# Performance work log

Measured on AMD Instinct MI355X. Metric: run time of the kernel, lower is better.

The kernel has to match this reference:

```python
import jax, jax.numpy as jnp
import numpy as np

N_LAYERS = 6
N_HEADS = 8
HIDDEN = 512
FILTER = 2048
KSIZE = 3
WINDOW = 10
DK = HIDDEN // N_HEADS


def _rel_to_abs(x):
    # x: [b, h, l, 2l-1] -> [b, h, l, l]
    b, h, l, _ = x.shape
    x = jnp.pad(x, ((0, 0), (0, 0), (0, 0), (0, 1)))
    x = x.reshape(b, h, l * 2 * l)
    x = jnp.pad(x, ((0, 0), (0, 0), (0, l - 1)))
    return x.reshape(b, h, l + 1, 2 * l - 1)[:, :, :l, l - 1:]


def _abs_to_rel(x):
    # x: [b, h, l, l] -> [b, h, l, 2l-1]
    b, h, l, _ = x.shape
    x = jnp.pad(x, ((0, 0), (0, 0), (0, 0), (0, l - 1)))
    x = x.reshape(b, h, l * l + l * (l - 1))
    x = jnp.pad(x, ((0, 0), (0, 0), (l, 0)))
    return x.reshape(b, h, l, 2 * l)[:, :, :, 1:]


def _get_rel_emb(emb, length):
    # emb: [1, 2w+1, dk] -> [1, 2*length-1, dk]  (static python ints)
    pad = max(length - (WINDOW + 1), 0)
    s = max(WINDOW + 1 - length, 0)
    e = s + 2 * length - 1
    emb = jnp.pad(emb, ((0, 0), (pad, pad), (0, 0)))
    return emb[:, s:e]


def _conv1x1(x, w, b):
    # x: [B, Cin, T], w: [Cout, Cin] -> [B, Cout, T]
    return jnp.einsum('oc,bct->bot', w, x) + b[None, :, None]


def _conv1d_same(x, w, b):
    # x: [B, Cin, T], w: [Cout, Cin, K], same padding (pad_l=(K-1)//2, pad_r=K//2)
    x = jnp.pad(x, ((0, 0), (0, 0), ((KSIZE - 1) // 2, KSIZE // 2)))
    y = jax.lax.conv_general_dilated(x, w, (1,), 'VALID',
                                     dimension_numbers=('NCH', 'OIH', 'NCH'))
    return y + b[None, :, None]


def _layer_norm(x, g, b):
    # normalize over channel axis (axis=1), eps=1e-5 (VITS LayerNorm)
    m = jnp.mean(x, axis=1, keepdims=True)
    v = jnp.var(x, axis=1, keepdims=True)
    return (x - m) * jax.lax.rsqrt(v + 1e-5) * g[None, :, None] + b[None, :, None]


def _mha(x, attn_mask, Wq, bq, Wk, bk, Wv, bv, Wo, bo, erk, erv):
    B, C, T = x.shape
    q = _conv1x1(x, Wq, bq)
    k = _conv1x1(x, Wk, bk)
    v = _conv1x1(x, Wv, bv)
    # [B, C, T] -> [B, H, T, Dk]
    def split_heads(t):
        return t.reshape(B, N_HEADS, DK, T).transpose(0, 1, 3, 2)
    q, k, v = split_heads(q), split_heads(k), split_heads(v)
    scale = 1.0 / np.sqrt(DK).astype(np.float32)
    scores = jnp.einsum('bhtd,bhsd->bhts', q * scale, k)
    # relative position logits
    rel_k = _get_rel_emb(erk, T)[0]                       # [2T-1, Dk]
    rel_logits = jnp.einsum('bhtd,rd->bhtr', q * scale, rel_k)
    scores = scores + _rel_to_abs(rel_logits)
    scores = jnp.where(attn_mask == 0, -1e4, scores)
    p = jax.nn.softmax(scores, axis=-1)
    out = jnp.einsum('bhts,bhsd->bhtd', p, v)
    rel_v = _get_rel_emb(erv, T)[0]                       # [2T-1, Dk]
    out = out + jnp.einsum('bhtr,rd->bhtd', _abs_to_rel(p), rel_v)
    out = out.transpose(0, 1, 3, 2).reshape(B, C, T)
    return _conv1x1(out, Wo, bo)


def _ffn(x, x_mask, W1, bf1, W2, bf2):
    y = _conv1d_same(x * x_mask, W1, bf1)
    y = jax.nn.relu(y)
    y = _conv1d_same(y * x_mask, W2, bf2)
    return y * x_mask


def reference(x, x_mask, Wq, bq, Wk, bk, Wv, bv, Wo, bo, erk, erv,
              g1, b1, g2, b2, W1, bf1, W2, bf2):
    attn_mask = x_mask[:, :, None, :] * x_mask[:, :, :, None]  # [B,1,T,T]
    x = x * x_mask
    for i in range(N_LAYERS):
        y = _mha(x, attn_mask, Wq[i], bq[i], Wk[i], bk[i], Wv[i], bv[i],
                 Wo[i], bo[i], erk[i], erv[i])
        x = _layer_norm(x + y, g1[i], b1[i])
        y = _ffn(x, x_mask, W1[i], bf1[i], W2[i], bf2[i])
        x = _layer_norm(x + y, g2[i], b2[i])
    return x * x_mask


def setup_inputs() -> dict:
    key = jax.random.key(0)
    ks = jax.random.split(key, 20)
    B, T = 8, 512
    xavier = lambda k, sh, fan: jax.random.normal(k, sh, jnp.float32) * np.sqrt(2.0 / fan).astype(np.float32)
    rel_std = DK ** -0.5
    return {
        'x': jax.random.normal(ks[0], (B, HIDDEN, T), jnp.float32),
        'x_mask': jnp.ones((B, 1, T), jnp.float32),
        'Wq': xavier(ks[1], (N_LAYERS, HIDDEN, HIDDEN), 2 * HIDDEN),
        'bq': jnp.zeros((N_LAYERS, HIDDEN), jnp.float32),
        'Wk': xavier(ks[2], (N_LAYERS, HIDDEN, HIDDEN), 2 * HIDDEN),
        'bk': jnp.zeros((N_LAYERS, HIDDEN), jnp.float32),
        'Wv': xavier(ks[3], (N_LAYERS, HIDDEN, HIDDEN), 2 * HIDDEN),
        'bv': jnp.zeros((N_LAYERS, HIDDEN), jnp.float32),
        'Wo': xavier(ks[4], (N_LAYERS, HIDDEN, HIDDEN), 2 * HIDDEN),
        'bo': jnp.zeros((N_LAYERS, HIDDEN), jnp.float32),
        'erk': jax.random.normal(ks[5], (N_LAYERS, 1, 2 * WINDOW + 1, DK), jnp.float32) * rel_std,
        'erv': jax.random.normal(ks[6], (N_LAYERS, 1, 2 * WINDOW + 1, DK), jnp.float32) * rel_std,
        'g1': jnp.ones((N_LAYERS, HIDDEN), jnp.float32),
        'b1': jnp.zeros((N_LAYERS, HIDDEN), jnp.float32),
        'g2': jnp.ones((N_LAYERS, HIDDEN), jnp.float32),
        'b2': jnp.zeros((N_LAYERS, HIDDEN), jnp.float32),
        'W1': jax.random.normal(ks[7], (N_LAYERS, FILTER, HIDDEN, KSIZE), jnp.float32) * np.sqrt(1.0 / (HIDDEN * KSIZE)).astype(np.float32),
        'bf1': jnp.zeros((N_LAYERS, FILTER), jnp.float32),
        'W2': jax.random.normal(ks[8], (N_LAYERS, HIDDEN, FILTER, KSIZE), jnp.float32) * np.sqrt(1.0 / (FILTER * KSIZE)).astype(np.float32),
        'bf2': jnp.zeros((N_LAYERS, HIDDEN), jnp.float32),
    }
```

## Files before the change

kernel.cpp:

```cpp
#include <hip/hip_runtime.h>


#define NLAYERS 6
#define BB 8
#define TT 512
#define CC 512
#define FF 2048
#define HH 8
#define DKK 64
#define WW 10

static_assert(CC == HH * DKK, "");

typedef __attribute__((ext_vector_type(8))) short short8;
typedef __attribute__((ext_vector_type(4))) float f32x4;
typedef unsigned short ushort;

#define BCTS ((size_t)BB * CC * TT)

__device__ __forceinline__ ushort f2bs(float f) {
    unsigned u = __float_as_uint(f);
    u = (u + 0x7FFFu + ((u >> 16) & 1u)) >> 16;
    return (ushort)u;
}
__device__ __forceinline__ float bf2f(ushort u) {
    return __uint_as_float(((unsigned)u) << 16);
}
__device__ __forceinline__ float wave_sum(float v) {
    #pragma unroll
    for (int off = 32; off > 0; off >>= 1) v += __shfl_xor(v, off, 64);
    return v;
}

__global__ __launch_bounds__(256) void init_trans(const float* __restrict__ in,
                                                  const float* __restrict__ mask,
                                                  float* __restrict__ xf,
                                                  ushort* __restrict__ xt) {
    __shared__ float tile[32][33];
    const int t0 = blockIdx.x * 32;
    const int c0 = blockIdx.y * 32;
    const int b = blockIdx.z;
    const int col = threadIdx.x & 31;
    const int row = threadIdx.x >> 5;
    const float* src = in + ((size_t)b * CC + c0) * TT + t0;
    #pragma unroll
    for (int r = 0; r < 32; r += 8)
        tile[row + r][col] = src[(size_t)(row + r) * TT + col];
    __syncthreads();
    #pragma unroll
    for (int r = 0; r < 32; r += 8) {
        const int t = t0 + row + r;
        const float mv = mask[b * TT + t];
        const float v = tile[col][row + r] * mv;
        const size_t idx = ((size_t)(b * TT) + t) * CC + c0 + col;
        xf[idx] = v;
        xt[idx] = f2bs(v);
    }
}

__global__ __launch_bounds__(256) void final_kernel(const float* __restrict__ xf,
                                                    const float* __restrict__ mask,
                                                    float* __restrict__ out) {
    __shared__ float tile[32][33];
    const int t0 = blockIdx.x * 32;
    const int c0 = blockIdx.y * 32;
    const int b = blockIdx.z;
    const int col = threadIdx.x & 31;
    const int row = threadIdx.x >> 5;
    #pragma unroll
    for (int r = 0; r < 32; r += 8)
        tile[row + r][col] = xf[((size_t)(b * TT) + t0 + row + r) * CC + c0 + col];
    __syncthreads();
    #pragma unroll
    for (int r = 0; r < 32; r += 8) {
        const int c = c0 + row + r;
        const int t = t0 + col;
        out[((size_t)b * CC + c) * TT + t] = tile[col][row + r] * mask[b * TT + t];
    }
}

__global__ __launch_bounds__(256) void wcvt_layer(const float* __restrict__ Wq,
                                                  const float* __restrict__ Wk,
                                                  const float* __restrict__ Wv,
                                                  const float* __restrict__ bq,
                                                  const float* __restrict__ bk,
                                                  const float* __restrict__ bv,
                                                  const float* __restrict__ Wo,
                                                  const float* __restrict__ W1,
                                                  const float* __restrict__ W2,
                                                  ushort* __restrict__ Wqkv,
                                                  float* __restrict__ bqkv,
                                                  ushort* __restrict__ Wot,
                                                  ushort* __restrict__ W1t,
                                                  ushort* __restrict__ W2t) {
    size_t i = (size_t)blockIdx.x * 256 + threadIdx.x;
    if (i < 1536)
        bqkv[i] = (i < 512) ? bq[i] : (i < 1024) ? bk[i - 512] : bv[i - 1024];
    if (i < 786432) {
        const int o = (int)(i >> 9), c = (int)(i & 511);
        const float* src = (o < 512) ? Wq : (o < 1024) ? Wk : Wv;
        Wqkv[i] = f2bs(src[(size_t)(o & 511) * 512 + c]);
        return;
    }
    i -= 786432;
    if (i < 262144) { Wot[i] = f2bs(Wo[i]); return; }
    i -= 262144;
    if (i < 3145728) {
        const int c = (int)(i & 511);
        const int o = (int)((i >> 9) & 2047);
        const int tap = (int)(i >> 20);
        W1t[i] = f2bs(W1[((size_t)o * 512 + c) * 3 + tap]);
        return;
    }
    i -= 3145728;
    if (i < 3145728) {
        const int c = (int)(i & 2047);
        const int o = (int)((i >> 11) & 511);
        const int tap = (int)(i >> 20);
        W2t[i] = f2bs(W2[((size_t)o * 2048 + c) * 3 + tap]);
    }
}

template <int MODE, int TN>
__global__ __launch_bounds__(256) void gemm128(const ushort* __restrict__ Wt,
                                               const float* __restrict__ bias,
                                               const ushort* __restrict__ Xin,
                                               void* __restrict__ Out,
                                               const float* __restrict__ mask,
                                               int O, int K, int taps, int kcs) {
    const int blk = blockIdx.x;
    const int b = blk >> 2;
    const int t0 = (blk & 3) * 128;
    const int o0 = blockIdx.y * TN;
    const int tid = threadIdx.x;
    const int wid = tid >> 6, lane = tid & 63, ln = lane & 15, q = lane >> 4;
    constexpr int MF = (TN == 128) ? 4 : 2;
    const int msub = (TN == 128) ? (wid & 1) * 64 : wid * 32;
    const int nsub = (TN == 128) ? (wid >> 1) * 64 : 0;

    __shared__ ushort Xs[128][40];
    __shared__ ushort Ws[TN][40];

    f32x4 acc[MF][4] = {};

    const int KC = K >> 5;
    const int NI = taps * KC;
    const int kcm = KC - 1;

    const int rx = tid >> 1;
    const int cx = (tid & 1) << 4;
    const int rw = (TN == 128) ? (tid >> 1) : (tid >> 2);
    const int cw = (TN == 128) ? ((tid & 1) << 4) : ((tid & 3) << 3);

    uint4 xr0, xr1, wr0, wr1;
    const uint4 zero = make_uint4(0u, 0u, 0u, 0u);

    auto load = [&](int it) {
        const int tap = it >> kcs;
        const int c0 = (it & kcm) << 5;
        const int shift = (taps > 1) ? (tap - 1) : 0;
        const int tt = t0 + rx + shift;
        const bool okt = (tt >= 0) && (tt < TT);
        const ushort* xp = Xin + ((size_t)(b * TT + (okt ? tt : 0)) * K + c0 + cx);
        xr0 = okt ? *(const uint4*)xp : zero;
        xr1 = okt ? *(const uint4*)(xp + 8) : zero;
        const ushort* wp = Wt + ((size_t)(tap * O + o0 + rw) * K + c0 + cw);
        wr0 = *(const uint4*)wp;
        if (TN == 128) wr1 = *(const uint4*)(wp + 8);
    };

    load(0);
    for (int it = 0; it < NI; ++it) {
        __syncthreads();
        *(uint4*)&Xs[rx][cx] = xr0;
        *(uint4*)&Xs[rx][cx + 8] = xr1;
        *(uint4*)&Ws[rw][cw] = wr0;
        if (TN == 128) *(uint4*)&Ws[rw][cw + 8] = wr1;
        if (it + 1 < NI) load(it + 1);
        __syncthreads();
        short8 afr[MF], bfr[4];
        #pragma unroll
        for (int mi = 0; mi < MF; ++mi)
            afr[mi] = *(const short8*)&Xs[msub + mi * 16 + ln][q * 8];
        #pragma unroll
        for (int ni = 0; ni < 4; ++ni)
            bfr[ni] = *(const short8*)&Ws[nsub + ni * 16 + ln][q * 8];
        #pragma unroll
        for (int mi = 0; mi < MF; ++mi)
            #pragma unroll
            for (int ni = 0; ni < 4; ++ni)
                acc[mi][ni] = __builtin_amdgcn_mfma_f32_16x16x32_bf16(
                    afr[mi], bfr[ni], acc[mi][ni], 0, 0, 0);
    }

    #pragma unroll
    for (int ni = 0; ni < 4; ++ni) {
        const int o = o0 + nsub + ni * 16 + ln;
        const float bv = bias[o];
        #pragma unroll
        for (int mi = 0; mi < MF; ++mi) {
            const int t = t0 + msub + mi * 16 + q * 4;
            if (MODE == 0) {
                float* Op = (float*)Out;
                #pragma unroll
                for (int r = 0; r < 4; ++r)
                    Op[((size_t)(b * TT) + t + r) * O + o] = acc[mi][ni][r] + bv;
            } else {
                ushort* Op = (ushort*)Out;
                const int which = o >> 9, oo = o & 511;
                if (which < 2) {
                    #pragma unroll
                    for (int r = 0; r < 4; ++r)
                        Op[(size_t)which * BCTS + ((size_t)(b * TT) + t + r) * CC + oo] =
                            f2bs(acc[mi][ni][r] + bv);
                } else {
                    ushort tmp[4];
                    #pragma unroll
                    for (int r = 0; r < 4; ++r) tmp[r] = f2bs(acc[mi][ni][r] + bv);
                    *(uint2*)&Op[2 * BCTS + ((size_t)(b * CC) + oo) * TT + t] =
                        *(const uint2*)tmp;
                }
            }
        }
    }
}

template <int TN, int KSPLIT, int MODE>
__global__ __launch_bounds__(256) void conv_gemm(const ushort* __restrict__ Wt,
                                                 const float* __restrict__ bias,
                                                 const ushort* __restrict__ Xin,
                                                 void* __restrict__ Out,
                                                 const float* __restrict__ mask,
                                                 int O, int K) {
    const int blk = blockIdx.x;
    const int b = blk >> 2;
    const int t0 = (blk & 3) * 128;
    const int o0 = blockIdx.y * TN;
    const int kz = (KSPLIT > 1) ? blockIdx.z : 0;
    const int tid = threadIdx.x;
    const int wid = tid >> 6, lane = tid & 63, ln = lane & 15, q = lane >> 4;
    constexpr int MF = (TN == 128) ? 4 : 2;
    constexpr int TSH = (TN == 128) ? 7 : 6;
    const int msub = (TN == 128) ? (wid & 1) * 64 : wid * 32;
    const int nsub = (TN == 128) ? (wid >> 1) * 64 : 0;

    __shared__ ushort Xs[130][40];
    __shared__ ushort Ws[3 * TN][40];

    f32x4 acc[MF][4] = {};

    const int Kc = K / KSPLIT;
    const int cbase = kz * Kc;
    const int NC = Kc >> 5;

    const int rx = tid >> 1;
    const int cx = (tid & 1) << 4;
    const int rw0 = tid >> 2;
    const int cw = (tid & 3) << 3;

    const ushort* Xb = Xin + (size_t)b * TT * K;

    for (int cc = 0; cc < NC; ++cc) {
        const int c0 = cbase + (cc << 5);
        __syncthreads();
        {
            const ushort* xp = Xb + (size_t)(t0 + rx) * K + c0 + cx;
            *(uint4*)&Xs[rx + 1][cx] = *(const uint4*)xp;
            *(uint4*)&Xs[rx + 1][cx + 8] = *(const uint4*)(xp + 8);
        }
        if (tid < 8) {
            const int hr = (tid < 4) ? -1 : 128;
            const int cu = (tid & 3) << 3;
            const int tg = t0 + hr;
            uint4 v = make_uint4(0u, 0u, 0u, 0u);
            if (tg >= 0 && tg < TT)
                v = *(const uint4*)(Xb + (size_t)tg * K + c0 + cu);
            *(uint4*)&Xs[hr + 1][cu] = v;
        }
        #pragma unroll
        for (int j = 0; j < 3 * TN / 64; ++j) {
            const int r = rw0 + j * 64;
            const int tap = r >> TSH, o = r & (TN - 1);
            const ushort* wp = Wt + ((size_t)(tap * O + o0 + o)) * K + c0 + cw;
            *(uint4*)&Ws[r][cw] = *(const uint4*)wp;
        }
        __syncthreads();
        #pragma unroll
        for (int tap = 0; tap < 3; ++tap) {
            short8 afr[MF], bfr[4];
            #pragma unroll
            for (int mi = 0; mi < MF; ++mi)
                afr[mi] = *(const short8*)&Xs[msub + mi * 16 + ln + tap][q * 8];
            #pragma unroll
            for (int ni = 0; ni < 4; ++ni)
                bfr[ni] = *(const short8*)&Ws[tap * TN + nsub + ni * 16 + ln][q * 8];
            #pragma unroll
            for (int mi = 0; mi < MF; ++mi)
                #pragma unroll
                for (int ni = 0; ni < 4; ++ni)
                    acc[mi][ni] = __builtin_amdgcn_mfma_f32_16x16x32_bf16(
                        afr[mi], bfr[ni], acc[mi][ni], 0, 0, 0);
        }
    }

    #pragma unroll
    for (int ni = 0; ni < 4; ++ni) {
        const int o = o0 + nsub + ni * 16 + ln;
        #pragma unroll
        for (int mi = 0; mi < MF; ++mi) {
            const int t = t0 + msub + mi * 16 + q * 4;
            if (MODE == 1) {
                const float bv = bias[o];
                ushort* Op = (ushort*)Out;
                #pragma unroll
                for (int r = 0; r < 4; ++r) {
                    float v = fmaxf(acc[mi][ni][r] + bv, 0.f) * mask[b * TT + t + r];
                    Op[((size_t)(b * TT) + t + r) * (size_t)O + o] = f2bs(v);
                }
            } else {
                float* Op = (float*)Out + (size_t)kz * BCTS;
                #pragma unroll
                for (int r = 0; r < 4; ++r)
                    Op[((size_t)(b * TT) + t + r) * O + o] = acc[mi][ni][r];
            }
        }
    }
}

__global__ __launch_bounds__(256) void fattn_kernel(const ushort* __restrict__ qkvt,
                                                    const float* __restrict__ mask,
                                                    const float* __restrict__ erk,
                                                    const float* __restrict__ erv,
                                                    ushort* __restrict__ xto) {
    const int t0 = blockIdx.x * 64;
    const int bh = blockIdx.y;
    const int b = bh >> 3, h = bh & 7;
    const int tid = threadIdx.x;
    const int wm = tid >> 6;
    const int lane = tid & 63;
    const int ln = lane & 15;
    const int q4 = lane >> 4;

    __shared__ ushort Qs[64][72];
    __shared__ ushort Ks[64][72];
    __shared__ ushort Vs[64][72];
    __shared__ ushort Ps[64][72];
    __shared__ float rel[64][2 * WW + 1];
    __shared__ float ervs[2 * WW + 1][DKK];
    __shared__ float mtile[64];
    __shared__ float mstile[64];

    const int sr = tid >> 2;
    const int sc = (tid & 3) << 4;

    {
        const ushort* qp = qkvt + ((size_t)(b * TT + t0 + sr) * CC + h * DKK + sc);
        *(uint4*)&Qs[sr][sc] = *(const uint4*)qp;
        *(uint4*)&Qs[sr][sc + 8] = *(const uint4*)(qp + 8);
    }
    if (tid < 64) mtile[tid] = mask[b * TT + t0 + tid];
    for (int idx = tid; idx < (2 * WW + 1) * DKK; idx += 256)
        ervs[idx / DKK][idx % DKK] = erv[idx];
    __syncthreads();

    for (int idx = tid; idx < 64 * (2 * WW + 1); idx += 256) {
        const int t = idx / (2 * WW + 1), w = idx % (2 * WW + 1);
        float s = 0.f;
        for (int d = 0; d < DKK; ++d)
            s += bf2f(Qs[t][d]) * erk[w * DKK + d];
        rel[t][w] = 0.125f * s;
    }
    __syncthreads();

    float m_run[4], l_run[4];
    #pragma unroll
    for (int r = 0; r < 4; ++r) { m_run[r] = -1e30f; l_run[r] = 0.f; }
    f32x4 Oacc[4] = {};
    f32x4 Racc[4] = {};

    for (int s0 = 0; s0 < TT; s0 += 64) {
        {
            const ushort* kp = qkvt + BCTS + ((size_t)(b * TT + s0 + sr) * CC + h * DKK + sc);
            *(uint4*)&Ks[sr][sc] = *(const uint4*)kp;
            *(uint4*)&Ks[sr][sc + 8] = *(const uint4*)(kp + 8);
            const ushort* vp = qkvt + 2 * BCTS + ((size_t)(b * CC + h * DKK + sr) * TT + s0 + sc);
            *(uint4*)&Vs[sr][sc] = *(const uint4*)vp;
            *(uint4*)&Vs[sr][sc + 8] = *(const uint4*)(vp + 8);
        }
        if (tid < 64) mstile[tid] = mask[b * TT + s0 + tid];
        __syncthreads();

        f32x4 accs[4] = {};
        {
            short8 a0 = *(const short8*)&Qs[wm * 16 + ln][q4 * 8];
            short8 a1 = *(const short8*)&Qs[wm * 16 + ln][32 + q4 * 8];
            #pragma unroll
            for (int ni = 0; ni < 4; ++ni) {
                short8 b0 = *(const short8*)&Ks[ni * 16 + ln][q4 * 8];
                short8 b1 = *(const short8*)&Ks[ni * 16 + ln][32 + q4 * 8];
                accs[ni] = __builtin_amdgcn_mfma_f32_16x16x32_bf16(a0, b0, accs[ni], 0, 0, 0);
                accs[ni] = __builtin_amdgcn_mfma_f32_16x16x32_bf16(a1, b1, accs[ni], 0, 0, 0);
            }
        }

        float mx[4];
        #pragma unroll
        for (int r = 0; r < 4; ++r) {
            const int tl = wm * 16 + q4 * 4 + r;
            const float mt = mtile[tl];
            float best = -1e30f;
            #pragma unroll
            for (int ni = 0; ni < 4; ++ni) {
                const int sl = ni * 16 + ln;
                const int wb = (s0 + sl) - (t0 + tl) + WW;
                float v = accs[ni][r] * 0.125f;
                if ((unsigned)wb <= 2u * WW) v += rel[tl][wb];
                if (mt * mstile[sl] == 0.f) v = -1e4f;
                accs[ni][r] = v;
                best = fmaxf(best, v);
            }
            #pragma unroll
            for (int off = 8; off >= 1; off >>= 1)
                best = fmaxf(best, __shfl_xor(best, off, 64));
            mx[r] = best;
        }

        #pragma unroll
        for (int r = 0; r < 4; ++r) {
            const float mnew = fmaxf(m_run[r], mx[r]);
            const float alpha = __expf(m_run[r] - mnew);
            m_run[r] = mnew;
            float rsum = 0.f;
            #pragma unroll
            for (int ni = 0; ni < 4; ++ni) {
                const float p = __expf(accs[ni][r] - mnew);
                accs[ni][r] = p;
                rsum += p;
            }
            #pragma unroll
            for (int off = 8; off >= 1; off >>= 1)
                rsum += __shfl_xor(rsum, off, 64);
            l_run[r] = l_run[r] * alpha + rsum;
            #pragma unroll
            for (int ni = 0; ni < 4; ++ni) {
                Oacc[ni][r] *= alpha;
                Racc[ni][r] *= alpha;
            }
        }

        #pragma unroll
        for (int ni = 0; ni < 4; ++ni)
            #pragma unroll
            for (int r = 0; r < 4; ++r)
                Ps[wm * 16 + q4 * 4 + r][ni * 16 + ln] = f2bs(accs[ni][r]);
        __syncthreads();

        {
            short8 a0 = *(const short8*)&Ps[wm * 16 + ln][q4 * 8];
            short8 a1 = *(const short8*)&Ps[wm * 16 + ln][32 + q4 * 8];
            #pragma unroll
            for (int ni = 0; ni < 4; ++ni) {
                short8 b0 = *(const short8*)&Vs[ni * 16 + ln][q4 * 8];
                short8 b1 = *(const short8*)&Vs[ni * 16 + ln][32 + q4 * 8];
                Oacc[ni] = __builtin_amdgcn_mfma_f32_16x16x32_bf16(a0, b0, Oacc[ni], 0, 0, 0);
                Oacc[ni] = __builtin_amdgcn_mfma_f32_16x16x32_bf16(a1, b1, Oacc[ni], 0, 0, 0);
            }
        }

        if (s0 + 63 >= t0 - WW && s0 <= t0 + 63 + WW) {
            #pragma unroll
            for (int r = 0; r < 4; ++r) {
                const int tl = wm * 16 + q4 * 4 + r;
                const int tg = t0 + tl;
                for (int w = 0; w <= 2 * WW; ++w) {
                    const int sl = tg + w - WW - s0;
                    if ((unsigned)sl < 64u) {
                        const float p = bf2f(Ps[tl][sl]);
                        #pragma unroll
                        for (int ni = 0; ni < 4; ++ni)
                            Racc[ni][r] += p * ervs[w][ni * 16 + ln];
                    }
                }
            }
        }
        __syncthreads();
    }

    #pragma unroll
    for (int ni = 0; ni < 4; ++ni) {
        const int d = ni * 16 + ln;
        #pragma unroll
        for (int r = 0; r < 4; ++r) {
            const int t = t0 + wm * 16 + q4 * 4 + r;
            xto[((size_t)(b * TT) + t) * CC + h * DKK + d] =
                f2bs((Oacc[ni][r] + Racc[ni][r]) / l_run[r]);
        }
    }
}

__global__ __launch_bounds__(256) void addln_kernel(float* __restrict__ x,
                                                    const float* __restrict__ p0,
                                                    const float* __restrict__ p1,
                                                    const float* __restrict__ biasc,
                                                    const float* __restrict__ g,
                                                    const float* __restrict__ bt,
                                                    const float* __restrict__ mask,
                                                    int maskY,
                                                    ushort* __restrict__ xtout,
                                                    int maskOut) {
    const int row = blockIdx.x * 4 + (threadIdx.x >> 6);
    const int lane = threadIdx.x & 63;
    const float m = mask[row];
    const float mv = maskY ? m : 1.f;
    const float mo = maskOut ? m : 1.f;
    const size_t base = (size_t)row * CC;
    const int c0 = lane * 8;

    f32x4 v0, v1;
    {
        f32x4 a0 = *(const f32x4*)(x + base + c0);
        f32x4 a1 = *(const f32x4*)(x + base + c0 + 4);
        f32x4 y0 = *(const f32x4*)(p0 + base + c0);
        f32x4 y1 = *(const f32x4*)(p0 + base + c0 + 4);
        if (p1) {
            f32x4 z0 = *(const f32x4*)(p1 + base + c0);
            f32x4 z1 = *(const f32x4*)(p1 + base + c0 + 4);
            #pragma unroll
            for (int r = 0; r < 4; ++r) { y0[r] += z0[r]; y1[r] += z1[r]; }
        }
        if (biasc) {
            f32x4 bc0 = *(const f32x4*)(biasc + c0);
            f32x4 bc1 = *(const f32x4*)(biasc + c0 + 4);
            #pragma unroll
            for (int r = 0; r < 4; ++r) { y0[r] += bc0[r]; y1[r] += bc1[r]; }
        }
        #pragma unroll
        for (int r = 0; r < 4; ++r) {
            v0[r] = a0[r] + y0[r] * mv;
            v1[r] = a1[r] + y1[r] * mv;
        }
    }

    float s = 0.f, s2 = 0.f;
    #pragma unroll
    for (int r = 0; r < 4; ++r) {
        s += v0[r] + v1[r];
        s2 += v0[r] * v0[r] + v1[r] * v1[r];
    }
    s = wave_sum(s);
    s2 = wave_sum(s2);
    const float mean = s * (1.f / CC);
    const float var = s2 * (1.f / CC) - mean * mean;
    const float rstd = rsqrtf(var + 1e-5f);

    f32x4 g0 = *(const f32x4*)(g + c0);
    f32x4 g1v = *(const f32x4*)(g + c0 + 4);
    f32x4 bt0 = *(const f32x4*)(bt + c0);
    f32x4 bt1 = *(const f32x4*)(bt + c0 + 4);
    f32x4 o0, o1;
    ushort ob[8];
    #pragma unroll
    for (int r = 0; r < 4; ++r) {
        o0[r] = (v0[r] - mean) * rstd * g0[r] + bt0[r];
        o1[r] = (v1[r] - mean) * rstd * g1v[r] + bt1[r];
        ob[r] = f2bs(o0[r] * mo);
        ob[4 + r] = f2bs(o1[r] * mo);
    }
    *(f32x4*)(x + base + c0) = o0;
    *(f32x4*)(x + base + c0 + 4) = o1;
    *(uint4*)(xtout + base + c0) = *(const uint4*)ob;
}

extern "C" void kernel_launch(void* const* d_in, const int* in_sizes, int n_in,
                              void* d_out, int out_size, void* d_ws, size_t ws_size,
                              hipStream_t stream) {
    const float* x_in = (const float*)d_in[0];
    const float* mask = (const float*)d_in[1];
    const float* Wq = (const float*)d_in[2];
    const float* bq = (const float*)d_in[3];
    const float* Wk = (const float*)d_in[4];
    const float* bk = (const float*)d_in[5];
    const float* Wv = (const float*)d_in[6];
    const float* bv = (const float*)d_in[7];
    const float* Wo = (const float*)d_in[8];
    const float* bo = (const float*)d_in[9];
    const float* erk = (const float*)d_in[10];
    const float* erv = (const float*)d_in[11];
    const float* g1 = (const float*)d_in[12];
    const float* b1 = (const float*)d_in[13];
    const float* g2 = (const float*)d_in[14];
    const float* b2 = (const float*)d_in[15];
    const float* W1 = (const float*)d_in[16];
    const float* bf1 = (const float*)d_in[17];
    const float* W2 = (const float*)d_in[18];
    const float* bf2 = (const float*)d_in[19];

    float* xf = (float*)d_ws;
    ushort* Xt = (ushort*)(xf + BCTS);
    ushort* qkvt = Xt + BCTS;
    ushort* Xto = qkvt + 3 * BCTS;
    float* parts = (float*)(Xto + BCTS);
    ushort* Midt = (ushort*)(parts + 2 * BCTS);
    ushort* Wqkv = Midt + 4 * BCTS;
    float* bqkv = (float*)(Wqkv + (size_t)1536 * 512);
    ushort* Wot = (ushort*)(bqkv + 1536);
    ushort* W1t = Wot + (size_t)CC * CC;
    ushort* W2t = W1t + (size_t)3 * FF * CC;

    init_trans<<<dim3(TT / 32, CC / 32, BB), 256, 0, stream>>>(x_in, mask, xf, Xt);

    const size_t nW = 786432 + 262144 + 3145728 + 3145728;
    const int wcvtBlocks = (int)((nW + 255) / 256);

    for (int L = 0; L < NLAYERS; ++L) {
        wcvt_layer<<<wcvtBlocks, 256, 0, stream>>>(
            Wq + (size_t)L * CC * CC, Wk + (size_t)L * CC * CC, Wv + (size_t)L * CC * CC,
            bq + (size_t)L * CC, bk + (size_t)L * CC, bv + (size_t)L * CC,
            Wo + (size_t)L * CC * CC,
            W1 + (size_t)L * 3 * FF * CC, W2 + (size_t)L * 3 * FF * CC,
            Wqkv, bqkv, Wot, W1t, W2t);

        gemm128<2, 128><<<dim3(32, 12), 256, 0, stream>>>(
            Wqkv, bqkv, Xt, qkvt, mask, 1536, CC, 1, 4);

        fattn_kernel<<<dim3(TT / 64, BB * HH), 256, 0, stream>>>(
            qkvt, mask, erk + (size_t)L * (2 * WW + 1) * DKK,
            erv + (size_t)L * (2 * WW + 1) * DKK, Xto);

        gemm128<0, 64><<<dim3(32, 8), 256, 0, stream>>>(
            Wot, bo + (size_t)L * CC, Xto, parts, mask, CC, CC, 1, 4);
        addln_kernel<<<BB * TT / 4, 256, 0, stream>>>(
            xf, parts, nullptr, nullptr,
            g1 + (size_t)L * CC, b1 + (size_t)L * CC, mask, 0, Xt, 1);

        conv_gemm<128, 1, 1><<<dim3(32, FF / 128, 1), 256, 0, stream>>>(
            W1t, bf1 + (size_t)L * FF, Xt, Midt, mask, FF, CC);
        conv_gemm<64, 2, 3><<<dim3(32, CC / 64, 2), 256, 0, stream>>>(
            W2t, nullptr, Midt, parts, mask, CC, FF);
        addln_kernel<<<BB * TT / 4, 256, 0, stream>>>(
            xf, parts, parts + BCTS, bf2 + (size_t)L * CC,
            g2 + (size_t)L * CC, b2 + (size_t)L * CC, mask, 1, Xt, 0);
    }

    final_kernel<<<dim3(TT / 32, CC / 32, BB), 256, 0, stream>>>(xf, mask, (float*)d_out);
}
```

Baseline: 1.413 ms.

## Split attention over key range with merge kernel and MFMA rel-key logits

The flash-attention kernel now splits the key sequence into two halves across a third grid dimension, writing unnormalized outputs plus per-row running max and sum to scratch buffers. A new merge kernel combines the two halves with softmax rescaling and writes the bf16 head output. The relative-key logits are now computed with MFMA against a bf16 copy of the embeddings instead of a scalar loop, Q fragments are hoisted into registers, and the P tile reuses the Q shared buffer. This doubles the number of attention blocks to fill more compute units, at the cost of an extra launch, extra fp32 scratch traffic and bf16 rounding of the relative embeddings.

```diff
diff --git a/kernel.cpp b/kernel.cpp
--- a/kernel.cpp
+++ b/kernel.cpp
@@ -9,6 +9,8 @@
 #define HH 8
 #define DKK 64
 #define WW 10
+#define SPLITS 2
+#define BHT (BB * HH * TT)
 
 static_assert(CC == HH * DKK, "");
 
@@ -331,9 +333,11 @@
                                                     const float* __restrict__ mask,
                                                     const float* __restrict__ erk,
                                                     const float* __restrict__ erv,
-                                                    ushort* __restrict__ xto) {
+                                                    float* __restrict__ Nacc,
+                                                    float* __restrict__ Ml) {
     const int t0 = blockIdx.x * 64;
     const int bh = blockIdx.y;
+    const int kz = blockIdx.z;
     const int b = bh >> 3, h = bh & 7;
     const int tid = threadIdx.x;
     const int wm = tid >> 6;
@@ -341,12 +345,11 @@
     const int ln = lane & 15;
     const int q4 = lane >> 4;
 
-    __shared__ ushort Qs[64][72];
+    __shared__ ushort QPs[64][72];
     __shared__ ushort Ks[64][72];
     __shared__ ushort Vs[64][72];
-    __shared__ ushort Ps[64][72];
     __shared__ float rel[64][2 * WW + 1];
-    __shared__ float ervs[2 * WW + 1][DKK];
+    __shared__ ushort ervs[2 * WW + 1][DKK];
     __shared__ float mtile[64];
     __shared__ float mstile[64];
 
@@ -355,20 +358,39 @@
 
     {
         const ushort* qp = qkvt + ((size_t)(b * TT + t0 + sr) * CC + h * DKK + sc);
-        *(uint4*)&Qs[sr][sc] = *(const uint4*)qp;
-        *(uint4*)&Qs[sr][sc + 8] = *(const uint4*)(qp + 8);
-    }
+        *(uint4*)&QPs[sr][sc] = *(const uint4*)qp;
+        *(uint4*)&QPs[sr][sc + 8] = *(const uint4*)(qp + 8);
+    }
+    for (int i = tid; i < 32 * DKK; i += 256) {
+        const int w = i >> 6, d = i & 63;
+        Vs[w][d] = (w < 2 * WW + 1) ? f2bs(erk[w * DKK + d]) : (ushort)0;
+    }
+    for (int i = tid; i < (2 * WW + 1) * DKK; i += 256)
+        ervs[i / DKK][i % DKK] = f2bs(erv[i]);
     if (tid < 64) mtile[tid] = mask[b * TT + t0 + tid];
-    for (int idx = tid; idx < (2 * WW + 1) * DKK; idx += 256)
-        ervs[idx / DKK][idx % DKK] = erv[idx];
     __syncthreads();
 
-    for (int idx = tid; idx < 64 * (2 * WW + 1); idx += 256) {
-        const int t = idx / (2 * WW + 1), w = idx % (2 * WW + 1);
-        float s = 0.f;
-        for (int d = 0; d < DKK; ++d)
-            s += bf2f(Qs[t][d]) * erk[w * DKK + d];
-        rel[t][w] = 0.125f * s;
+    const short8 a0 = *(const short8*)&QPs[wm * 16 + ln][q4 * 8];
+    const short8 a1 = *(const short8*)&QPs[wm * 16 + ln][32 + q4 * 8];
+
+    {
+        f32x4 ra[2] = {};
+        #pragma unroll
+        for (int ni = 0; ni < 2; ++ni) {
+            short8 b0 = *(const short8*)&Vs[ni * 16 + ln][q4 * 8];
+            short8 b1 = *(const short8*)&Vs[ni * 16 + ln][32 + q4 * 8];
+            ra[ni] = __builtin_amdgcn_mfma_f32_16x16x32_bf16(a0, b0, ra[ni], 0, 0, 0);
+            ra[ni] = __builtin_amdgcn_mfma_f32_16x16x32_bf16(a1, b1, ra[ni], 0, 0, 0);
+        }
+        #pragma unroll
+        for (int ni = 0; ni < 2; ++ni) {
+            const int col = ni * 16 + ln;
+            if (col < 2 * WW + 1) {
+                #pragma unroll
+                for (int r = 0; r < 4; ++r)
+                    rel[wm * 16 + q4 * 4 + r][col] = ra[ni][r] * 0.125f;
+            }
+        }
     }
     __syncthreads();
 
@@ -378,7 +400,9 @@
     f32x4 Oacc[4] = {};
     f32x4 Racc[4] = {};
 
-    for (int s0 = 0; s0 < TT; s0 += 64) {
+    const int sbeg = kz * (TT / SPLITS);
+    const int send = sbeg + TT / SPLITS;
+    for (int s0 = sbeg; s0 < send; s0 += 64) {
         {
             const ushort* kp = qkvt + BCTS + ((size_t)(b * TT + s0 + sr) * CC + h * DKK + sc);
             *(uint4*)&Ks[sr][sc] = *(const uint4*)kp;
@@ -392,8 +416,6 @@
 
         f32x4 accs[4] = {};
         {
-            short8 a0 = *(const short8*)&Qs[wm * 16 + ln][q4 * 8];
-            short8 a1 = *(const short8*)&Qs[wm * 16 + ln][32 + q4 * 8];
             #pragma unroll
             for (int ni = 0; ni < 4; ++ni) {
                 short8 b0 = *(const short8*)&Ks[ni * 16 + ln][q4 * 8];
@@ -452,18 +474,18 @@
         for (int ni = 0; ni < 4; ++ni)
             #pragma unroll
             for (int r = 0; r < 4; ++r)
-                Ps[wm * 16 + q4 * 4 + r][ni * 16 + ln] = f2bs(accs[ni][r]);
+                QPs[wm * 16 + q4 * 4 + r][ni * 16 + ln] = f2bs(accs[ni][r]);
         __syncthreads();
 
         {
-            short8 a0 = *(const short8*)&Ps[wm * 16 + ln][q4 * 8];
-            short8 a1 = *(const short8*)&Ps[wm * 16 + ln][32 + q4 * 8];
+            short8 p0 = *(const short8*)&QPs[wm * 16 + ln][q4 * 8];
+            short8 p1 = *(const short8*)&QPs[wm * 16 + ln][32 + q4 * 8];
             #pragma unroll
             for (int ni = 0; ni < 4; ++ni) {
                 short8 b0 = *(const short8*)&Vs[ni * 16 + ln][q4 * 8];
                 short8 b1 = *(const short8*)&Vs[ni * 16 + ln][32 + q4 * 8];
-                Oacc[ni] = __builtin_amdgcn_mfma_f32_16x16x32_bf16(a0, b0, Oacc[ni], 0, 0, 0);
-                Oacc[ni] = __builtin_amdgcn_mfma_f32_16x16x32_bf16(a1, b1, Oacc[ni], 0, 0, 0);
+                Oacc[ni] = __builtin_amdgcn_mfma_f32_16x16x32_bf16(p0, b0, Oacc[ni], 0, 0, 0);
+                Oacc[ni] = __builtin_amdgcn_mfma_f32_16x16x32_bf16(p1, b1, Oacc[ni], 0, 0, 0);
             }
         }
 
@@ -475,10 +497,10 @@
                 for (int w = 0; w <= 2 * WW; ++w) {
                     const int sl = tg + w - WW - s0;
                     if ((unsigned)sl < 64u) {
-                        const float p = bf2f(Ps[tl][sl]);
+                        const float p = bf2f(QPs[tl][sl]);
                         #pragma unroll
                         for (int ni = 0; ni < 4; ++ni)
-                            Racc[ni][r] += p * ervs[w][ni * 16 + ln];
+                            Racc[ni][r] += p * bf2f(ervs[w][ni * 16 + ln]);
                     }
                 }
             }
@@ -486,16 +508,53 @@
         __syncthreads();
     }
 
+    const int rowb = (b * HH + h) * TT;
+    float* Np = Nacc + (size_t)kz * BHT * 64;
     #pragma unroll
     for (int ni = 0; ni < 4; ++ni) {
         const int d = ni * 16 + ln;
         #pragma unroll
         for (int r = 0; r < 4; ++r) {
             const int t = t0 + wm * 16 + q4 * 4 + r;
-            xto[((size_t)(b * TT) + t) * CC + h * DKK + d] =
-                f2bs((Oacc[ni][r] + Racc[ni][r]) / l_run[r]);
-        }
-    }
+            Np[(size_t)(rowb + t) * 64 + d] = Oacc[ni][r] + Racc[ni][r];
+        }
+    }
+    if (ln == 0) {
+        #pragma unroll
+        for (int r = 0; r < 4; ++r) {
+            const int t = t0 + wm * 16 + q4 * 4 + r;
+            Ml[(size_t)kz * BHT + rowb + t] = m_run[r];
+            Ml[(size_t)(SPLITS + kz) * BHT + rowb + t] = l_run[r];
+        }
+    }
+}
+
+__global__ __launch_bounds__(256) void fmerge_kernel(const float* __restrict__ Nacc,
+                                                     const float* __restrict__ Ml,
+                                                     ushort* __restrict__ xto) {
+    const int gid = blockIdx.x * 256 + threadIdx.x;
+    const int row = gid >> 3;
+    const int d0 = (gid & 7) << 3;
+    const float m0 = Ml[row], m1 = Ml[BHT + row];
+    const float l0 = Ml[2 * BHT + row], l1 = Ml[3 * BHT + row];
+    const float m = fmaxf(m0, m1);
+    const float e0 = __expf(m0 - m), e1 = __expf(m1 - m);
+    const float inv = 1.f / (l0 * e0 + l1 * e1);
+    const float w0 = e0 * inv, w1 = e1 * inv;
+    const float* n0 = Nacc + (size_t)row * 64 + d0;
+    const float* n1 = n0 + (size_t)BHT * 64;
+    f32x4 x0 = *(const f32x4*)n0, x1 = *(const f32x4*)(n0 + 4);
+    f32x4 y0 = *(const f32x4*)n1, y1 = *(const f32x4*)(n1 + 4);
+    ushort ob[8];
+    #pragma unroll
+    for (int r = 0; r < 4; ++r) {
+        ob[r] = f2bs(x0[r] * w0 + y0[r] * w1);
+        ob[4 + r] = f2bs(x1[r] * w0 + y1[r] * w1);
+    }
+    const int t = row & (TT - 1);
+    const int h = (row >> 9) & 7;
+    const int bb = row >> 12;
+    *(uint4*)&xto[((size_t)(bb * TT + t)) * CC + h * DKK + d0] = *(const uint4*)ob;
 }
 
 __global__ __launch_bounds__(256) void addln_kernel(float* __restrict__ x,
@@ -623,9 +682,11 @@
         gemm128<2, 128><<<dim3(32, 12), 256, 0, stream>>>(
             Wqkv, bqkv, Xt, qkvt, mask, 1536, CC, 1, 4);
 
-        fattn_kernel<<<dim3(TT / 64, BB * HH), 256, 0, stream>>>(
+        fattn_kernel<<<dim3(TT / 64, BB * HH, SPLITS), 256, 0, stream>>>(
             qkvt, mask, erk + (size_t)L * (2 * WW + 1) * DKK,
-            erv + (size_t)L * (2 * WW + 1) * DKK, Xto);
+            erv + (size_t)L * (2 * WW + 1) * DKK, parts, (float*)Midt);
+        fmerge_kernel<<<BHT * 8 / 256, 256, 0, stream>>>(
+            parts, (const float*)Midt, Xto);
 
         gemm128<0, 64><<<dim3(32, 8), 256, 0, stream>>>(
             Wot, bo + (size_t)L * CC, Xto, parts, mask, CC, CC, 1, 4);
```

After: 1.403 ms. About the same (-0.7%).

## Restructure relative-position flash attention into independent per-wave tiles without block syncs

Applied to the files above, without the earlier changes.

The attention kernel now gives each wave its own 16 query rows and streams K and V directly from global memory into MFMA operands in 32-key steps, replacing the shared-memory K/V tiles and the per-tile __syncthreads. The relative-key logits are computed with MFMA instead of a scalar loop. Pre-softmax banded scores are kept in shared memory and the relative-value term is applied once at the end using the final max, instead of accumulating it inside the loop. The aim is to remove block-level barriers and LDS staging, at the cost of redundant global loads of K/V across the four waves and reliance on cache hits.

```diff
diff --git a/kernel.cpp b/kernel.cpp
--- a/kernel.cpp
+++ b/kernel.cpp
@@ -332,169 +332,175 @@
                                                     const float* __restrict__ erk,
                                                     const float* __restrict__ erv,
                                                     ushort* __restrict__ xto) {
-    const int t0 = blockIdx.x * 64;
-    const int bh = blockIdx.y;
-    const int b = bh >> 3, h = bh & 7;
     const int tid = threadIdx.x;
     const int wm = tid >> 6;
     const int lane = tid & 63;
     const int ln = lane & 15;
     const int q4 = lane >> 4;
-
-    __shared__ ushort Qs[64][72];
-    __shared__ ushort Ks[64][72];
-    __shared__ ushort Vs[64][72];
-    __shared__ ushort Ps[64][72];
-    __shared__ float rel[64][2 * WW + 1];
+    const int bh = blockIdx.y;
+    const int b = bh >> 3, h = bh & 7;
+    const int t0g = blockIdx.x * 64 + wm * 16;
+
     __shared__ float ervs[2 * WW + 1][DKK];
-    __shared__ float mtile[64];
-    __shared__ float mstile[64];
-
-    const int sr = tid >> 2;
-    const int sc = (tid & 3) << 4;
+    __shared__ float msS[TT];
+    __shared__ float relS[4][16][22];
+    __shared__ float band[4][16][24];
+    __shared__ ushort Pt[4][16][40];
+
+    for (int i = tid; i < (2 * WW + 1) * DKK; i += 256)
+        ervs[i / DKK][i % DKK] = erv[i];
+    for (int i = tid; i < TT; i += 256)
+        msS[i] = mask[b * TT + i];
+
+    #pragma unroll
+    for (int i = 0; i < 6; ++i) {
+        const int idx = lane + i * 64;
+        ((float*)band[wm])[idx] = -1e30f;
+    }
+
+    const ushort* qrow = qkvt + ((size_t)(b * TT + t0g + ln) * CC + h * DKK);
+    const short8 qb0 = *(const short8*)(qrow + q4 * 8);
+    const short8 qb1 = *(const short8*)(qrow + 32 + q4 * 8);
 
     {
-        const ushort* qp = qkvt + ((size_t)(b * TT + t0 + sr) * CC + h * DKK + sc);
-        *(uint4*)&Qs[sr][sc] = *(const uint4*)qp;
-        *(uint4*)&Qs[sr][sc + 8] = *(const uint4*)(qp + 8);
-    }
-    if (tid < 64) mtile[tid] = mask[b * TT + t0 + tid];
-    for (int idx = tid; idx < (2 * WW + 1) * DKK; idx += 256)
-        ervs[idx / DKK][idx % DKK] = erv[idx];
+        const float* ekL = erk;
+        short8 ea0, ea1;
+        {
+            const float* ep = ekL + ln * DKK + q4 * 8;
+            #pragma unroll
+            for (int j = 0; j < 8; ++j) ea0[j] = (short)f2bs(ep[j]);
+            #pragma unroll
+            for (int j = 0; j < 8; ++j) ea1[j] = (short)f2bs(ep[32 + j]);
+        }
+        f32x4 c0 = {};
+        c0 = __builtin_amdgcn_mfma_f32_16x16x32_bf16(ea0, qb0, c0, 0, 0, 0);
+        c0 = __builtin_amdgcn_mfma_f32_16x16x32_bf16(ea1, qb1, c0, 0, 0, 0);
+        #pragma unroll
+        for (int r = 0; r < 4; ++r)
+            relS[wm][ln][q4 * 4 + r] = c0[r] * 0.125f;
+        short8 eb0 = {}, eb1 = {};
+        if (ln < 2 * WW + 1 - 16) {
+            const float* ep = ekL + (16 + ln) * DKK + q4 * 8;
+            #pragma unroll
+            for (int j = 0; j < 8; ++j) eb0[j] = (short)f2bs(ep[j]);
+            #pragma unroll
+            for (int j = 0; j < 8; ++j) eb1[j] = (short)f2bs(ep[32 + j]);
+        }
+        f32x4 c1 = {};
+        c1 = __builtin_amdgcn_mfma_f32_16x16x32_bf16(eb0, qb0, c1, 0, 0, 0);
+        c1 = __builtin_amdgcn_mfma_f32_16x16x32_bf16(eb1, qb1, c1, 0, 0, 0);
+        #pragma unroll
+        for (int r = 0; r < 4; ++r) {
+            const int w = 16 + q4 * 4 + r;
+            if (w < 2 * WW + 1) relS[wm][ln][w] = c1[r] * 0.125f;
+        }
+    }
+
     __syncthreads();
 
-    for (int idx = tid; idx < 64 * (2 * WW + 1); idx += 256) {
-        const int t = idx / (2 * WW + 1), w = idx % (2 * WW + 1);
-        float s = 0.f;
-        for (int d = 0; d < DKK; ++d)
-            s += bf2f(Qs[t][d]) * erk[w * DKK + d];
-        rel[t][w] = 0.125f * s;
-    }
-    __syncthreads();
-
-    float m_run[4], l_run[4];
-    #pragma unroll
-    for (int r = 0; r < 4; ++r) { m_run[r] = -1e30f; l_run[r] = 0.f; }
+    const float mt = msS[t0g + ln];
+
+    float m_run = -1e30f, l_run = 0.f;
     f32x4 Oacc[4] = {};
-    f32x4 Racc[4] = {};
-
-    for (int s0 = 0; s0 < TT; s0 += 64) {
-        {
-            const ushort* kp = qkvt + BCTS + ((size_t)(b * TT + s0 + sr) * CC + h * DKK + sc);
-            *(uint4*)&Ks[sr][sc] = *(const uint4*)kp;
-            *(uint4*)&Ks[sr][sc + 8] = *(const uint4*)(kp + 8);
-            const ushort* vp = qkvt + 2 * BCTS + ((size_t)(b * CC + h * DKK + sr) * TT + s0 + sc);
-            *(uint4*)&Vs[sr][sc] = *(const uint4*)vp;
-            *(uint4*)&Vs[sr][sc + 8] = *(const uint4*)(vp + 8);
-        }
-        if (tid < 64) mstile[tid] = mask[b * TT + s0 + tid];
-        __syncthreads();
-
-        f32x4 accs[4] = {};
-        {
-            short8 a0 = *(const short8*)&Qs[wm * 16 + ln][q4 * 8];
-            short8 a1 = *(const short8*)&Qs[wm * 16 + ln][32 + q4 * 8];
-            #pragma unroll
-            for (int ni = 0; ni < 4; ++ni) {
-                short8 b0 = *(const short8*)&Ks[ni * 16 + ln][q4 * 8];
-                short8 b1 = *(const short8*)&Ks[ni * 16 + ln][32 + q4 * 8];
-                accs[ni] = __builtin_amdgcn_mfma_f32_16x16x32_bf16(a0, b0, accs[ni], 0, 0, 0);
-                accs[ni] = __builtin_amdgcn_mfma_f32_16x16x32_bf16(a1, b1, accs[ni], 0, 0, 0);
+
+    const ushort* Kbase = qkvt + BCTS + ((size_t)(b * TT) * CC + h * DKK);
+    const ushort* Vbase = qkvt + 2 * BCTS + ((size_t)(b * CC + h * DKK) * TT);
+
+    for (int s0 = 0; s0 < TT; s0 += 32) {
+        const ushort* klo = Kbase + (size_t)(s0 + ln) * CC;
+        const ushort* khi = klo + 16 * CC;
+        const short8 ka0 = *(const short8*)(klo + q4 * 8);
+        const short8 ka1 = *(const short8*)(klo + 32 + q4 * 8);
+        const short8 kb0 = *(const short8*)(khi + q4 * 8);
+        const short8 kb1 = *(const short8*)(khi + 32 + q4 * 8);
+
+        f32x4 slo = {}, shi = {};
+        slo = __builtin_amdgcn_mfma_f32_16x16x32_bf16(ka0, qb0, slo, 0, 0, 0);
+        slo = __builtin_amdgcn_mfma_f32_16x16x32_bf16(ka1, qb1, slo, 0, 0, 0);
+        shi = __builtin_amdgcn_mfma_f32_16x16x32_bf16(kb0, qb0, shi, 0, 0, 0);
+        shi = __builtin_amdgcn_mfma_f32_16x16x32_bf16(kb1, qb1, shi, 0, 0, 0);
+
+        float v[2][4];
+        float bmax = -1e30f;
+        const int tg = t0g + ln;
+        #pragma unroll
+        for (int half = 0; half < 2; ++half) {
+            #pragma unroll
+            for (int r = 0; r < 4; ++r) {
+                const int s = s0 + half * 16 + q4 * 4 + r;
+                const int wb = s - tg + WW;
+                float vv = (half ? shi[r] : slo[r]) * 0.125f;
+                if ((unsigned)wb <= 2u * WW) vv += relS[wm][ln][wb];
+                if (mt * msS[s] == 0.f) vv = -1e4f;
+                if ((unsigned)wb <= 2u * WW) band[wm][ln][wb] = vv;
+                v[half][r] = vv;
+                bmax = fmaxf(bmax, vv);
             }
         }
-
-        float mx[4];
+        bmax = fmaxf(bmax, __shfl_xor(bmax, 16, 64));
+        bmax = fmaxf(bmax, __shfl_xor(bmax, 32, 64));
+
+        const float mnew = fmaxf(m_run, bmax);
+        const float alpha = __expf(m_run - mnew);
+        m_run = mnew;
+
+        float rsum = 0.f;
+        ushort pb[8];
+        #pragma unroll
+        for (int half = 0; half < 2; ++half)
+            #pragma unroll
+            for (int r = 0; r < 4; ++r) {
+                const float p = __expf(v[half][r] - mnew);
+                rsum += p;
+                pb[half * 4 + r] = f2bs(p);
+            }
+        rsum += __shfl_xor(rsum, 16, 64);
+        rsum += __shfl_xor(rsum, 32, 64);
+        l_run = l_run * alpha + rsum;
+
+        *(uint2*)&Pt[wm][ln][q4 * 4] = *(const uint2*)&pb[0];
+        *(uint2*)&Pt[wm][ln][16 + q4 * 4] = *(const uint2*)&pb[4];
+
         #pragma unroll
         for (int r = 0; r < 4; ++r) {
-            const int tl = wm * 16 + q4 * 4 + r;
-            const float mt = mtile[tl];
-            float best = -1e30f;
-            #pragma unroll
-            for (int ni = 0; ni < 4; ++ni) {
-                const int sl = ni * 16 + ln;
-                const int wb = (s0 + sl) - (t0 + tl) + WW;
-                float v = accs[ni][r] * 0.125f;
-                if ((unsigned)wb <= 2u * WW) v += rel[tl][wb];
-                if (mt * mstile[sl] == 0.f) v = -1e4f;
-                accs[ni][r] = v;
-                best = fmaxf(best, v);
-            }
-            #pragma unroll
-            for (int off = 8; off >= 1; off >>= 1)
-                best = fmaxf(best, __shfl_xor(best, off, 64));
-            mx[r] = best;
-        }
-
+            const float alr = __shfl(alpha, q4 * 4 + r, 64);
+            #pragma unroll
+            for (int dt = 0; dt < 4; ++dt) Oacc[dt][r] *= alr;
+        }
+
+        const short8 pa = *(const short8*)&Pt[wm][ln][q4 * 8];
+        #pragma unroll
+        for (int dt = 0; dt < 4; ++dt) {
+            const short8 vb = *(const short8*)(Vbase + (size_t)(dt * 16 + ln) * TT + s0 + q4 * 8);
+            Oacc[dt] = __builtin_amdgcn_mfma_f32_16x16x32_bf16(pa, vb, Oacc[dt], 0, 0, 0);
+        }
+    }
+
+    float mr[4], invl[4];
+    #pragma unroll
+    for (int r = 0; r < 4; ++r) {
+        mr[r] = __shfl(m_run, q4 * 4 + r, 64);
+        invl[r] = 1.f / __shfl(l_run, q4 * 4 + r, 64);
+    }
+    f32x4 racc[4] = {};
+    for (int w = 0; w <= 2 * WW; ++w) {
+        float ev[4];
+        #pragma unroll
+        for (int dt = 0; dt < 4; ++dt) ev[dt] = ervs[w][dt * 16 + ln];
         #pragma unroll
         for (int r = 0; r < 4; ++r) {
-            const float mnew = fmaxf(m_run[r], mx[r]);
-            const float alpha = __expf(m_run[r] - mnew);
-            m_run[r] = mnew;
-            float rsum = 0.f;
-            #pragma unroll
-            for (int ni = 0; ni < 4; ++ni) {
-                const float p = __expf(accs[ni][r] - mnew);
-                accs[ni][r] = p;
-                rsum += p;
-            }
-            #pragma unroll
-            for (int off = 8; off >= 1; off >>= 1)
-                rsum += __shfl_xor(rsum, off, 64);
-            l_run[r] = l_run[r] * alpha + rsum;
-            #pragma unroll
-            for (int ni = 0; ni < 4; ++ni) {
-                Oacc[ni][r] *= alpha;
-                Racc[ni][r] *= alpha;
-            }
-        }
-
-        #pragma unroll
-        for (int ni = 0; ni < 4; ++ni)
-            #pragma unroll
-            for (int r = 0; r < 4; ++r)
-                Ps[wm * 16 + q4 * 4 + r][ni * 16 + ln] = f2bs(accs[ni][r]);
-        __syncthreads();
-
-        {
-            short8 a0 = *(const short8*)&Ps[wm * 16 + ln][q4 * 8];
-            short8 a1 = *(const short8*)&Ps[wm * 16 + ln][32 + q4 * 8];
-            #pragma unroll
-            for (int ni = 0; ni < 4; ++ni) {
-                short8 b0 = *(const short8*)&Vs[ni * 16 + ln][q4 * 8];
-                short8 b1 = *(const short8*)&Vs[ni * 16 + ln][32 + q4 * 8];
-                Oacc[ni] = __builtin_amdgcn_mfma_f32_16x16x32_bf16(a0, b0, Oacc[ni], 0, 0, 0);
-                Oacc[ni] = __builtin_amdgcn_mfma_f32_16x16x32_bf16(a1, b1, Oacc[ni], 0, 0, 0);
-            }
-        }
-
-        if (s0 + 63 >= t0 - WW && s0 <= t0 + 63 + WW) {
-            #pragma unroll
-            for (int r = 0; r < 4; ++r) {
-                const int tl = wm * 16 + q4 * 4 + r;
-                const int tg = t0 + tl;
-                for (int w = 0; w <= 2 * WW; ++w) {
-                    const int sl = tg + w - WW - s0;
-                    if ((unsigned)sl < 64u) {
-                        const float p = bf2f(Ps[tl][sl]);
-                        #pragma unroll
-                        for (int ni = 0; ni < 4; ++ni)
-                            Racc[ni][r] += p * ervs[w][ni * 16 + ln];
-                    }
-                }
-            }
-        }
-        __syncthreads();
-    }
-
-    #pragma unroll
-    for (int ni = 0; ni < 4; ++ni) {
-        const int d = ni * 16 + ln;
-        #pragma unroll
-        for (int r = 0; r < 4; ++r) {
-            const int t = t0 + wm * 16 + q4 * 4 + r;
-            xto[((size_t)(b * TT) + t) * CC + h * DKK + d] =
-                f2bs((Oacc[ni][r] + Racc[ni][r]) / l_run[r]);
-        }
+            const float pw = __expf(band[wm][q4 * 4 + r][w] - mr[r]);
+            #pragma unroll
+            for (int dt = 0; dt < 4; ++dt) racc[dt][r] += pw * ev[dt];
+        }
+    }
+    #pragma unroll
+    for (int r = 0; r < 4; ++r) {
+        const int t = t0g + q4 * 4 + r;
+        #pragma unroll
+        for (int dt = 0; dt < 4; ++dt)
+            xto[((size_t)(b * TT) + t) * CC + h * DKK + dt * 16 + ln] =
+                f2bs((Oacc[dt][r] + racc[dt][r]) * invl[r]);
     }
 }
 
```

After: 1.260 ms. -10.8%, faster.
